# Optimization experiments

Hardware: AMD Instinct MI355X
Metric: run time of the kernel (lower is better)

Reference implementation:

```python
import jax, jax.numpy as jnp
import numpy as np

N = 100_000
E = 1_600_000
D_IN, D_H, D_L = 128, 64, 32


def _glorot(key, shape):
    fan_in, fan_out = shape[0], shape[1]
    s = jnp.sqrt(6.0 / (fan_in + fan_out)).astype(jnp.float32)
    return jax.random.uniform(key, shape, jnp.float32, -s, s)


def setup_inputs() -> dict:
    key = jax.random.key(0)
    ks = jax.random.split(key, 8)
    x = jax.random.normal(ks[0], (N, D_IN), jnp.float32)
    edge_index = jax.random.randint(ks[1], (2, E), 0, N, dtype=jnp.int64)
    return {
        "x": x,
        "edge_index": edge_index,
        "W1": _glorot(ks[2], (D_IN, D_H)),
        "b1": jnp.zeros((D_H,), jnp.float32),
        "W2": _glorot(ks[3], (D_H, D_L)),
        "b2": jnp.zeros((D_L,), jnp.float32),
        "Wd1": _glorot(ks[4], (D_L, D_H)),
        "bd1": jnp.zeros((D_H,), jnp.float32),
        "Wd2": _glorot(ks[5], (D_H, D_IN)),
        "bd2": jnp.zeros((D_IN,), jnp.float32),
    }


def gcn_conv(x, W, b, src, dst, num_nodes):
    """PyG GCNConv: add self-loops, symmetric normalization, aggregate, bias."""
    loop = jnp.arange(num_nodes, dtype=src.dtype)
    s = jnp.concatenate([src, loop])  # sources (message senders)
    d = jnp.concatenate([dst, loop])  # targets (message receivers)
    deg = jax.ops.segment_sum(jnp.ones_like(s, dtype=x.dtype), d, num_segments=num_nodes)
    dinv = jnp.where(deg > 0, jax.lax.rsqrt(deg), 0.0)
    norm = dinv[s] * dinv[d]                      # [E+N]
    h = x @ W                                     # [N, out] dense transform first
    msgs = h[s] * norm[:, None]                   # gather + scale, [E+N, out]
    out = jax.ops.segment_sum(msgs, d, num_segments=num_nodes)  # scatter-add
    return out + b


def reference(x, edge_index, W1, b1, W2, b2, Wd1, bd1, Wd2, bd2):
    src, dst = edge_index[0], edge_index[1]
    n = x.shape[0]
    z = gcn_conv(x, W1, b1, src, dst, n)
    z = jax.nn.relu(z)
    z = gcn_conv(z, W2, b2, src, dst, n)          # latent embedding
    h = jax.nn.relu(z @ Wd1 + bd1)
    reconstructed_x = h @ Wd2 + bd2
    return (reconstructed_x, z)
```

## Files before the change

### kernel.cpp

```cpp
#include <hip/hip_runtime.h>
#include <stdint.h>

#define N_NODES 100000
#define N_EDGES 1600000
#define D_INF   128
#define D_HID   64
#define D_LAT   32

typedef __attribute__((ext_vector_type(8))) short bf16x8;
typedef __attribute__((ext_vector_type(4))) float f32x4;
typedef __attribute__((ext_vector_type(8))) unsigned short u16x8;

__device__ __forceinline__ unsigned short f2bf(float v) {
  union { float f; unsigned int u; } x; x.f = v;
  unsigned int u = x.u + 0x7FFF + ((x.u >> 16) & 1);
  return (unsigned short)(u >> 16);
}
__device__ __forceinline__ float bf2f(unsigned short h) {
  union { unsigned int u; float f; } x; x.u = ((unsigned int)h) << 16;
  return x.f;
}


#define NBKT      196
#define BKT_SHIFT 9
#define BKT_CAP   10240
#define EPB       2048
#define ABLOCKS   782

__global__ __launch_bounds__(256) void k_binA(const int* __restrict__ esrc,
                                              const int* __restrict__ edst,
                                              int* __restrict__ bkcnt,
                                              int* __restrict__ stage) {
  __shared__ int cnt[NBKT];
  __shared__ int sc[256];
  __shared__ int garel[NBKT];
  __shared__ int pos[NBKT];
  __shared__ __align__(16) int2 stg[EPB];
  int t = threadIdx.x;
  int e0 = blockIdx.x * EPB;

  for (int i = t; i < NBKT; i += 256) cnt[i] = 0;
  __syncthreads();

  int ds[8], ss[8];
  const int4* s4 = (const int4*)esrc;
  const int4* d4 = (const int4*)edst;
#pragma unroll
  for (int i = 0; i < 2; i++) {
    int idx4 = (e0 >> 2) + i * 256 + t;
    int4 dd = make_int4(-1, -1, -1, -1);
    int4 sv = make_int4(0, 0, 0, 0);
    if (idx4 < N_EDGES / 4) { dd = d4[idx4]; sv = s4[idx4]; }
    ds[i*4+0] = dd.x; ds[i*4+1] = dd.y; ds[i*4+2] = dd.z; ds[i*4+3] = dd.w;
    ss[i*4+0] = sv.x; ss[i*4+1] = sv.y; ss[i*4+2] = sv.z; ss[i*4+3] = sv.w;
  }
#pragma unroll
  for (int j = 0; j < 8; j++)
    if (ds[j] >= 0) atomicAdd(&cnt[ds[j] >> BKT_SHIFT], 1);
  __syncthreads();

  int c = (t < NBKT) ? cnt[t] : 0;
  sc[t] = c;
  __syncthreads();
  int incl = c;
#pragma unroll
  for (int off = 1; off < 256; off <<= 1) {
    int x = (t >= off) ? sc[t - off] : 0;
    __syncthreads();
    incl += x;
    sc[t] = incl;
    __syncthreads();
  }
  if (t < NBKT) {
    int lb = incl - c;
    int gb = 0;
    if (c > 0) gb = t * BKT_CAP + atomicAdd(&bkcnt[t], c);
    garel[t] = gb - lb;
    pos[t]   = lb;
  }
  __syncthreads();

#pragma unroll
  for (int j = 0; j < 8; j++) {
    if (ds[j] >= 0) {
      int b  = ds[j] >> BKT_SHIFT;
      int lp = atomicAdd(&pos[b], 1);
      stg[lp] = make_int2(ss[j], ds[j]);
    }
  }
  __syncthreads();

  int nval = N_EDGES - e0; if (nval > EPB) nval = EPB;
  for (int i = t; i < nval; i += 256) {
    int2 e = stg[i];
    stage[garel[e.y >> BKT_SHIFT] + i] = (e.x << BKT_SHIFT) | (e.y & 511);
  }
}

__global__ __launch_bounds__(1024) void k_csr(const int* __restrict__ stage,
                                              const int* __restrict__ bkcnt,
                                              int* __restrict__ beg,
                                              int* __restrict__ cnt,
                                              float* __restrict__ dinv,
                                              int* __restrict__ csr4) {
  __shared__ int hist[512];
  __shared__ int scan[512];
  int b = blockIdx.x, t = threadIdx.x;
  if (t < 512) hist[t] = 0;
  __syncthreads();
  int n = bkcnt[b];
  int nlo = b << BKT_SHIFT;
  const int* reg = stage + (size_t)b * BKT_CAP;
  for (int i = t; i < n; i += 1024)
    atomicAdd(&hist[reg[i] & 511], 1);
  __syncthreads();
  int v = (t < 512) ? hist[t] : 0;
  if (t < 512) scan[t] = v;
  __syncthreads();
  int incl = v;
#pragma unroll
  for (int off = 1; off < 512; off <<= 1) {
    int x = (t >= off && t < 512) ? scan[t - off] : 0;
    __syncthreads();
    if (t < 512) { incl += x; scan[t] = incl; }
    __syncthreads();
  }
  if (t < 512) {
    int loc = incl - v;
    int node = nlo + t;
    if (node < N_NODES) {
      beg[node]  = b * BKT_CAP + loc;
      cnt[node]  = v;
      dinv[node] = rsqrtf((float)(v + 1));
    }
    scan[t] = loc;
  }
  __syncthreads();
  int* c4 = csr4 + (size_t)b * BKT_CAP;
  for (int i = t; i < n; i += 1024) {
    int e = reg[i];
    int slot = atomicAdd(&scan[e & 511], 1);
    c4[slot] = e >> BKT_SHIFT;
  }
}


__global__ void k_prep_w(const float* __restrict__ W1, const float* __restrict__ W2,
                         const float* __restrict__ Wd1, const float* __restrict__ Wd2,
                         unsigned short* __restrict__ w1hi, unsigned short* __restrict__ w1lo,
                         unsigned short* __restrict__ w2hi, unsigned short* __restrict__ w2lo,
                         unsigned short* __restrict__ wd1hi, unsigned short* __restrict__ wd1lo,
                         unsigned short* __restrict__ wd2hi, unsigned short* __restrict__ wd2lo,
                         int* __restrict__ bkcnt) {
  if (blockIdx.x == 4) {
    if (threadIdx.x < NBKT) bkcnt[threadIdx.x] = 0;
    return;
  }
  const float* src; unsigned short *hi, *lo; int K, M;
  switch (blockIdx.x) {
    case 0:  src = W1;  hi = w1hi;  lo = w1lo;  K = 128; M = 64;  break;
    case 1:  src = W2;  hi = w2hi;  lo = w2lo;  K = 64;  M = 32;  break;
    case 2:  src = Wd1; hi = wd1hi; lo = wd1lo; K = 32;  M = 64;  break;
    default: src = Wd2; hi = wd2hi; lo = wd2lo; K = 64;  M = 128; break;
  }
  int KP = K + 8;
  for (int i = threadIdx.x; i < K * M; i += 256) {
    int k = i / M, c = i % M;
    float v = src[i];
    unsigned short h = f2bf(v);
    hi[c * KP + k] = h;
    lo[c * KP + k] = f2bf(v - bf2f(h));
  }
}


template<int NODES, int K, int M>
__global__ __launch_bounds__(256) void k_mfma_gemm(const float* __restrict__ X,
                                                   const unsigned short* __restrict__ Bhi,
                                                   const unsigned short* __restrict__ Blo,
                                                   const float* __restrict__ dinv,
                                                   unsigned short* __restrict__ Y16) {
  constexpr int KP     = K + 8;
  constexpr int NSTRIP = M / 16;
  constexpr int KSTEPS = K / 32;
  constexpr int MTW    = (NODES / 16) * NSTRIP / 4;
  __shared__ __align__(16) unsigned short Ahi[NODES * KP];
  __shared__ __align__(16) unsigned short Alo[NODES * KP];

  int t = threadIdx.x;
  int node0 = blockIdx.x * NODES;

  for (int i = t; i < NODES * K / 4; i += 256) {
    int n = i / (K / 4), f4 = i % (K / 4);
    float4 v = make_float4(0.f, 0.f, 0.f, 0.f);
    if (node0 + n < N_NODES) v = ((const float4*)(X + (size_t)(node0 + n) * K))[f4];
    int base = n * KP + f4 * 4;
    float vv[4] = {v.x, v.y, v.z, v.w};
#pragma unroll
    for (int j = 0; j < 4; j++) {
      unsigned short h = f2bf(vv[j]);
      Ahi[base + j] = h;
      Alo[base + j] = f2bf(vv[j] - bf2f(h));
    }
  }
  __syncthreads();

  int w = t >> 6, lane = t & 63;
  int quad = lane >> 4, r16 = lane & 15;
  int strip = w % NSTRIP;

  bf16x8 bh[KSTEPS], bl[KSTEPS];
  const unsigned short* bp = Bhi + (strip * 16 + r16) * KP + quad * 8;
  const unsigned short* bq = Blo + (strip * 16 + r16) * KP + quad * 8;
#pragma unroll
  for (int ks = 0; ks < KSTEPS; ks++) {
    bh[ks] = *(const bf16x8*)(bp + ks * 32);
    bl[ks] = *(const bf16x8*)(bq + ks * 32);
  }

#pragma unroll
  for (int c = 0; c < MTW; c++) {
    int mt = (w / NSTRIP) * MTW + c;
    f32x4 acc = {0.f, 0.f, 0.f, 0.f};
    const unsigned short* ap = &Ahi[(mt * 16 + r16) * KP + quad * 8];
    const unsigned short* aq = &Alo[(mt * 16 + r16) * KP + quad * 8];
#pragma unroll
    for (int ks = 0; ks < KSTEPS; ks++) {
      bf16x8 ah = *(const bf16x8*)(ap + ks * 32);
      bf16x8 al = *(const bf16x8*)(aq + ks * 32);
      acc = __builtin_amdgcn_mfma_f32_16x16x32_bf16(ah, bh[ks], acc, 0, 0, 0);
      acc = __builtin_amdgcn_mfma_f32_16x16x32_bf16(ah, bl[ks], acc, 0, 0, 0);
      acc = __builtin_amdgcn_mfma_f32_16x16x32_bf16(al, bh[ks], acc, 0, 0, 0);
    }
    int gn  = node0 + mt * 16 + quad * 4;
    int col = strip * 16 + r16;
#pragma unroll
    for (int r = 0; r < 4; r++) {
      if (gn + r < N_NODES)
        Y16[(size_t)(gn + r) * M + col] = f2bf(acc[r] * dinv[gn + r]);
    }
  }
}


template<int FEAT, bool RELU>
__global__ __launch_bounds__(256) void k_aggregate(const unsigned short* __restrict__ H16,
                            const int* __restrict__ beg,
                            const int* __restrict__ cnt,
                            const int* __restrict__ csr4,
                            const float* __restrict__ dinv, const float* __restrict__ bias,
                            float* __restrict__ OUT) {
  constexpr int LPE    = FEAT / 8;
  constexpr int GROUPS = 64 / LPE;

  int node = blockIdx.x * 4 + (threadIdx.x >> 6);
  int lane = threadIdx.x & 63;
  if (node >= N_NODES) return;
  int bg = beg[node], end = bg + cnt[node];
  int g  = lane / LPE;
  int f8 = lane % LPE;

  float a0=0.f,a1=0.f,a2=0.f,a3=0.f,a4=0.f,a5=0.f,a6=0.f,a7=0.f;

  for (int p = bg; p < end; p += 4 * GROUPS) {
    int   sarr[4];
    float marr[4];
    u16x8 harr[4];
#pragma unroll
    for (int b4 = 0; b4 < 4; b4++) {
      int q = p + b4 * GROUPS + g;
      sarr[b4] = (q < end) ? csr4[q] : node;
      marr[b4] = (q < end) ? 1.f : 0.f;
    }
#pragma unroll
    for (int b4 = 0; b4 < 4; b4++)
      harr[b4] = *(const u16x8*)(H16 + (size_t)sarr[b4] * FEAT + f8 * 8);
#pragma unroll
    for (int b4 = 0; b4 < 4; b4++) {
      float m = marr[b4];
      u16x8 h = harr[b4];
      a0 += bf2f(h[0]) * m; a1 += bf2f(h[1]) * m;
      a2 += bf2f(h[2]) * m; a3 += bf2f(h[3]) * m;
      a4 += bf2f(h[4]) * m; a5 += bf2f(h[5]) * m;
      a6 += bf2f(h[6]) * m; a7 += bf2f(h[7]) * m;
    }
  }

#pragma unroll
  for (int off = LPE; off < 64; off <<= 1) {
    a0 += __shfl_xor(a0, off, 64);
    a1 += __shfl_xor(a1, off, 64);
    a2 += __shfl_xor(a2, off, 64);
    a3 += __shfl_xor(a3, off, 64);
    a4 += __shfl_xor(a4, off, 64);
    a5 += __shfl_xor(a5, off, 64);
    a6 += __shfl_xor(a6, off, 64);
    a7 += __shfl_xor(a7, off, 64);
  }

  if (g == 0) {
    float di = dinv[node];
    u16x8 hs = *(const u16x8*)(H16 + (size_t)node * FEAT + f8 * 8);
    float4 bv0 = *(const float4*)(bias + f8 * 8);
    float4 bv1 = *(const float4*)(bias + f8 * 8 + 4);
    a0 = (a0 + bf2f(hs[0])) * di + bv0.x;
    a1 = (a1 + bf2f(hs[1])) * di + bv0.y;
    a2 = (a2 + bf2f(hs[2])) * di + bv0.z;
    a3 = (a3 + bf2f(hs[3])) * di + bv0.w;
    a4 = (a4 + bf2f(hs[4])) * di + bv1.x;
    a5 = (a5 + bf2f(hs[5])) * di + bv1.y;
    a6 = (a6 + bf2f(hs[6])) * di + bv1.z;
    a7 = (a7 + bf2f(hs[7])) * di + bv1.w;
    if (RELU) {
      a0 = fmaxf(a0, 0.f); a1 = fmaxf(a1, 0.f);
      a2 = fmaxf(a2, 0.f); a3 = fmaxf(a3, 0.f);
      a4 = fmaxf(a4, 0.f); a5 = fmaxf(a5, 0.f);
      a6 = fmaxf(a6, 0.f); a7 = fmaxf(a7, 0.f);
    }
    float4 o0; o0.x = a0; o0.y = a1; o0.z = a2; o0.w = a3;
    float4 o1; o1.x = a4; o1.y = a5; o1.z = a6; o1.w = a7;
    *(float4*)(OUT + (size_t)node * FEAT + f8 * 8)     = o0;
    *(float4*)(OUT + (size_t)node * FEAT + f8 * 8 + 4) = o1;
  }
}


__global__ __launch_bounds__(256) void k_decoder_mfma(
    const float* __restrict__ Z,
    const unsigned short* __restrict__ B1hi, const unsigned short* __restrict__ B1lo,
    const float* __restrict__ bd1,
    const unsigned short* __restrict__ B2hi, const unsigned short* __restrict__ B2lo,
    const float* __restrict__ bd2, float* __restrict__ RECON) {
  constexpr int KP1 = 40;
  constexpr int KP2 = 72;
  __shared__ __align__(16) unsigned short Azhi[64 * KP1];
  __shared__ __align__(16) unsigned short Azlo[64 * KP1];
  __shared__ __align__(16) unsigned short H3hi[64 * KP2];
  __shared__ __align__(16) unsigned short H3lo[64 * KP2];
  int t = threadIdx.x;
  int node0 = blockIdx.x * 64;

  for (int i = t; i < 512; i += 256) {
    int n = i >> 3, f4 = i & 7;
    float4 v = make_float4(0.f, 0.f, 0.f, 0.f);
    if (node0 + n < N_NODES) v = ((const float4*)(Z + (size_t)(node0 + n) * 32))[f4];
    int base = n * KP1 + f4 * 4;
    float vv[4] = {v.x, v.y, v.z, v.w};
#pragma unroll
    for (int j = 0; j < 4; j++) {
      unsigned short h = f2bf(vv[j]);
      Azhi[base + j] = h;
      Azlo[base + j] = f2bf(vv[j] - bf2f(h));
    }
  }
  __syncthreads();

  int w = t >> 6, lane = t & 63;
  int quad = lane >> 4, r16 = lane & 15;

  {
    int col = w * 16 + r16;
    float bias1 = bd1[col];
    bf16x8 bh = *(const bf16x8*)(B1hi + col * KP1 + quad * 8);
    bf16x8 bl = *(const bf16x8*)(B1lo + col * KP1 + quad * 8);
#pragma unroll
    for (int m = 0; m < 4; m++) {
      bf16x8 ah = *(const bf16x8*)(Azhi + (m * 16 + r16) * KP1 + quad * 8);
      bf16x8 al = *(const bf16x8*)(Azlo + (m * 16 + r16) * KP1 + quad * 8);
      f32x4 acc = {0.f, 0.f, 0.f, 0.f};
      acc = __builtin_amdgcn_mfma_f32_16x16x32_bf16(ah, bh, acc, 0, 0, 0);
      acc = __builtin_amdgcn_mfma_f32_16x16x32_bf16(ah, bl, acc, 0, 0, 0);
      acc = __builtin_amdgcn_mfma_f32_16x16x32_bf16(al, bh, acc, 0, 0, 0);
#pragma unroll
      for (int r = 0; r < 4; r++) {
        int row = m * 16 + quad * 4 + r;
        float hv = fmaxf(acc[r] + bias1, 0.f);
        unsigned short h = f2bf(hv);
        H3hi[row * KP2 + col] = h;
        H3lo[row * KP2 + col] = f2bf(hv - bf2f(h));
      }
    }
  }
  __syncthreads();

#pragma unroll
  for (int sp = 0; sp < 2; sp++) {
    int strip = w + sp * 4;
    int col = strip * 16 + r16;
    float bias2 = bd2[col];
    const unsigned short* b2h = B2hi + col * KP2 + quad * 8;
    const unsigned short* b2l = B2lo + col * KP2 + quad * 8;
    bf16x8 bh0 = *(const bf16x8*)(b2h);
    bf16x8 bh1 = *(const bf16x8*)(b2h + 32);
    bf16x8 bl0 = *(const bf16x8*)(b2l);
    bf16x8 bl1 = *(const bf16x8*)(b2l + 32);
#pragma unroll
    for (int m = 0; m < 4; m++) {
      const unsigned short* ahp = H3hi + (m * 16 + r16) * KP2 + quad * 8;
      const unsigned short* alp = H3lo + (m * 16 + r16) * KP2 + quad * 8;
      bf16x8 ah0 = *(const bf16x8*)(ahp);
      bf16x8 ah1 = *(const bf16x8*)(ahp + 32);
      bf16x8 al0 = *(const bf16x8*)(alp);
      bf16x8 al1 = *(const bf16x8*)(alp + 32);
      f32x4 acc = {0.f, 0.f, 0.f, 0.f};
      acc = __builtin_amdgcn_mfma_f32_16x16x32_bf16(ah0, bh0, acc, 0, 0, 0);
      acc = __builtin_amdgcn_mfma_f32_16x16x32_bf16(ah1, bh1, acc, 0, 0, 0);
      acc = __builtin_amdgcn_mfma_f32_16x16x32_bf16(ah0, bl0, acc, 0, 0, 0);
      acc = __builtin_amdgcn_mfma_f32_16x16x32_bf16(ah1, bl1, acc, 0, 0, 0);
      acc = __builtin_amdgcn_mfma_f32_16x16x32_bf16(al0, bh0, acc, 0, 0, 0);
      acc = __builtin_amdgcn_mfma_f32_16x16x32_bf16(al1, bh1, acc, 0, 0, 0);
#pragma unroll
      for (int r = 0; r < 4; r++) {
        int n = node0 + m * 16 + quad * 4 + r;
        if (n < N_NODES) RECON[(size_t)n * 128 + col] = acc[r] + bias2;
      }
    }
  }
}


extern "C" void kernel_launch(void* const* d_in, const int* in_sizes, int n_in,
                              void* d_out, int out_size, void* d_ws, size_t ws_size,
                              hipStream_t stream) {
  const float* x    = (const float*)d_in[0];
  const int*   eidx = (const int*)d_in[1];
  const int*   esrc = eidx;
  const int*   edst = eidx + N_EDGES;
  const float* W1  = (const float*)d_in[2];
  const float* b1  = (const float*)d_in[3];
  const float* W2  = (const float*)d_in[4];
  const float* b2  = (const float*)d_in[5];
  const float* Wd1 = (const float*)d_in[6];
  const float* bd1 = (const float*)d_in[7];
  const float* Wd2 = (const float*)d_in[8];
  const float* bd2 = (const float*)d_in[9];

  float* recon = (float*)d_out;
  float* z     = (float*)d_out + (size_t)N_NODES * D_INF;
  int*            stage = (int*)recon;
  unsigned short* h1_16 = (unsigned short*)recon;
  float*          z1    = (float*)((char*)recon + 12800000);
  unsigned short* h2_16 = (unsigned short*)((char*)recon + 38400000);

  char* ws = (char*)d_ws;
  int*   beg    = (int*)(ws + 0);
  int*   cntn   = (int*)(ws + 409600);
  float* dinv   = (float*)(ws + 819200);
  int*   bkcnt  = (int*)(ws + 1228800);
  int*   csr4   = (int*)(ws + 1229824);
  unsigned short* w1hi  = (unsigned short*)(ws + 9257984);
  unsigned short* w1lo  = (unsigned short*)(ws + 9275392);
  unsigned short* w2hi  = (unsigned short*)(ws + 9292800);
  unsigned short* w2lo  = (unsigned short*)(ws + 9297408);
  unsigned short* wd1hi = (unsigned short*)(ws + 9302016);
  unsigned short* wd1lo = (unsigned short*)(ws + 9307136);
  unsigned short* wd2hi = (unsigned short*)(ws + 9312256);
  unsigned short* wd2lo = (unsigned short*)(ws + 9330688);

  k_prep_w<<<5, 256, 0, stream>>>(W1, W2, Wd1, Wd2, w1hi, w1lo, w2hi, w2lo,
                                  wd1hi, wd1lo, wd2hi, wd2lo, bkcnt);
  k_binA<<<ABLOCKS, 256, 0, stream>>>(esrc, edst, bkcnt, stage);
  k_csr<<<NBKT, 1024, 0, stream>>>(stage, bkcnt, beg, cntn, dinv, csr4);

  k_mfma_gemm<64, 128, 64><<<(N_NODES + 63) / 64, 256, 0, stream>>>(x, w1hi, w1lo, dinv, h1_16);
  k_aggregate<64, true><<<(N_NODES + 3) / 4, 256, 0, stream>>>(h1_16, beg, cntn, csr4, dinv, b1, z1);
  k_mfma_gemm<64, 64, 32><<<(N_NODES + 63) / 64, 256, 0, stream>>>(z1, w2hi, w2lo, dinv, h2_16);
  k_aggregate<32, false><<<(N_NODES + 3) / 4, 256, 0, stream>>>(h2_16, beg, cntn, csr4, dinv, b2, z);
  k_decoder_mfma<<<(N_NODES + 63) / 64, 256, 0, stream>>>(z, wd1hi, wd1lo, bd1,
                                                          wd2hi, wd2lo, bd2, recon);
}
```

Baseline: 291.1 us.

## Fuse aggregation with following GEMM and decoder into two kernels

Merges the first GCN aggregation with the second layer's dense transform, and the second aggregation with the MLP decoder. Aggregated rows go to shared memory instead of global memory, which removes the fp32 z1 write and read and the z reread between kernels. The h2 buffer moves into the workspace, and the bucket capacity shrinks to make room for it. In exchange, each block now handles 64 nodes with 4 waves looping over 16 rows each, which may lower gather parallelism and occupancy. The tighter bucket capacity could also overflow on skewed degree distributions.

```diff
diff --git a/kernel.cpp b/kernel.cpp
--- a/kernel.cpp
+++ b/kernel.cpp
@@ -24,7 +24,7 @@
 
 #define NBKT      196
 #define BKT_SHIFT 9
-#define BKT_CAP   10240
+#define BKT_CAP   9216
 #define EPB       2048
 #define ABLOCKS   782
 
@@ -244,126 +244,208 @@
 }
 
 
-template<int FEAT, bool RELU>
-__global__ __launch_bounds__(256) void k_aggregate(const unsigned short* __restrict__ H16,
-                            const int* __restrict__ beg,
-                            const int* __restrict__ cnt,
-                            const int* __restrict__ csr4,
-                            const float* __restrict__ dinv, const float* __restrict__ bias,
-                            float* __restrict__ OUT) {
-  constexpr int LPE    = FEAT / 8;
-  constexpr int GROUPS = 64 / LPE;
-
-  int node = blockIdx.x * 4 + (threadIdx.x >> 6);
-  int lane = threadIdx.x & 63;
-  if (node >= N_NODES) return;
-  int bg = beg[node], end = bg + cnt[node];
-  int g  = lane / LPE;
-  int f8 = lane % LPE;
-
-  float a0=0.f,a1=0.f,a2=0.f,a3=0.f,a4=0.f,a5=0.f,a6=0.f,a7=0.f;
-
-  for (int p = bg; p < end; p += 4 * GROUPS) {
-    int   sarr[4];
-    float marr[4];
-    u16x8 harr[4];
-#pragma unroll
-    for (int b4 = 0; b4 < 4; b4++) {
-      int q = p + b4 * GROUPS + g;
-      sarr[b4] = (q < end) ? csr4[q] : node;
-      marr[b4] = (q < end) ? 1.f : 0.f;
-    }
-#pragma unroll
-    for (int b4 = 0; b4 < 4; b4++)
-      harr[b4] = *(const u16x8*)(H16 + (size_t)sarr[b4] * FEAT + f8 * 8);
-#pragma unroll
-    for (int b4 = 0; b4 < 4; b4++) {
-      float m = marr[b4];
-      u16x8 h = harr[b4];
-      a0 += bf2f(h[0]) * m; a1 += bf2f(h[1]) * m;
-      a2 += bf2f(h[2]) * m; a3 += bf2f(h[3]) * m;
-      a4 += bf2f(h[4]) * m; a5 += bf2f(h[5]) * m;
-      a6 += bf2f(h[6]) * m; a7 += bf2f(h[7]) * m;
-    }
-  }
-
-#pragma unroll
-  for (int off = LPE; off < 64; off <<= 1) {
-    a0 += __shfl_xor(a0, off, 64);
-    a1 += __shfl_xor(a1, off, 64);
-    a2 += __shfl_xor(a2, off, 64);
-    a3 += __shfl_xor(a3, off, 64);
-    a4 += __shfl_xor(a4, off, 64);
-    a5 += __shfl_xor(a5, off, 64);
-    a6 += __shfl_xor(a6, off, 64);
-    a7 += __shfl_xor(a7, off, 64);
-  }
-
-  if (g == 0) {
-    float di = dinv[node];
-    u16x8 hs = *(const u16x8*)(H16 + (size_t)node * FEAT + f8 * 8);
-    float4 bv0 = *(const float4*)(bias + f8 * 8);
-    float4 bv1 = *(const float4*)(bias + f8 * 8 + 4);
-    a0 = (a0 + bf2f(hs[0])) * di + bv0.x;
-    a1 = (a1 + bf2f(hs[1])) * di + bv0.y;
-    a2 = (a2 + bf2f(hs[2])) * di + bv0.z;
-    a3 = (a3 + bf2f(hs[3])) * di + bv0.w;
-    a4 = (a4 + bf2f(hs[4])) * di + bv1.x;
-    a5 = (a5 + bf2f(hs[5])) * di + bv1.y;
-    a6 = (a6 + bf2f(hs[6])) * di + bv1.z;
-    a7 = (a7 + bf2f(hs[7])) * di + bv1.w;
-    if (RELU) {
-      a0 = fmaxf(a0, 0.f); a1 = fmaxf(a1, 0.f);
-      a2 = fmaxf(a2, 0.f); a3 = fmaxf(a3, 0.f);
-      a4 = fmaxf(a4, 0.f); a5 = fmaxf(a5, 0.f);
-      a6 = fmaxf(a6, 0.f); a7 = fmaxf(a7, 0.f);
-    }
-    float4 o0; o0.x = a0; o0.y = a1; o0.z = a2; o0.w = a3;
-    float4 o1; o1.x = a4; o1.y = a5; o1.z = a6; o1.w = a7;
-    *(float4*)(OUT + (size_t)node * FEAT + f8 * 8)     = o0;
-    *(float4*)(OUT + (size_t)node * FEAT + f8 * 8 + 4) = o1;
-  }
-}
-
-
-__global__ __launch_bounds__(256) void k_decoder_mfma(
-    const float* __restrict__ Z,
-    const unsigned short* __restrict__ B1hi, const unsigned short* __restrict__ B1lo,
+__global__ __launch_bounds__(256) void k_agg1_gemm2(
+    const unsigned short* __restrict__ H16,
+    const int* __restrict__ beg, const int* __restrict__ cnt,
+    const int* __restrict__ csr4,
+    const float* __restrict__ dinv, const float* __restrict__ bias,
+    const unsigned short* __restrict__ B2hi, const unsigned short* __restrict__ B2lo,
+    unsigned short* __restrict__ H2) {
+  constexpr int KP = 72;
+  __shared__ __align__(16) unsigned short Azhi[64 * KP];
+  __shared__ __align__(16) unsigned short Azlo[64 * KP];
+  int t = threadIdx.x, w = t >> 6, lane = t & 63;
+  int node0 = blockIdx.x * 64;
+  int g = lane >> 3, f8 = lane & 7;
+
+  for (int it = 0; it < 16; ++it) {
+    int row  = it * 4 + w;
+    int node = node0 + row;
+    float a0=0.f,a1=0.f,a2=0.f,a3=0.f,a4=0.f,a5=0.f,a6=0.f,a7=0.f;
+    if (node < N_NODES) {
+      int bg = beg[node], end = bg + cnt[node];
+      for (int p = bg; p < end; p += 32) {
+        int   sarr[4]; float marr[4]; u16x8 harr[4];
+#pragma unroll
+        for (int b4 = 0; b4 < 4; b4++) {
+          int q = p + b4 * 8 + g;
+          sarr[b4] = (q < end) ? csr4[q] : node;
+          marr[b4] = (q < end) ? 1.f : 0.f;
+        }
+#pragma unroll
+        for (int b4 = 0; b4 < 4; b4++)
+          harr[b4] = *(const u16x8*)(H16 + (size_t)sarr[b4] * 64 + f8 * 8);
+#pragma unroll
+        for (int b4 = 0; b4 < 4; b4++) {
+          float m = marr[b4]; u16x8 h = harr[b4];
+          a0 += bf2f(h[0]) * m; a1 += bf2f(h[1]) * m;
+          a2 += bf2f(h[2]) * m; a3 += bf2f(h[3]) * m;
+          a4 += bf2f(h[4]) * m; a5 += bf2f(h[5]) * m;
+          a6 += bf2f(h[6]) * m; a7 += bf2f(h[7]) * m;
+        }
+      }
+#pragma unroll
+      for (int off = 8; off < 64; off <<= 1) {
+        a0 += __shfl_xor(a0, off, 64); a1 += __shfl_xor(a1, off, 64);
+        a2 += __shfl_xor(a2, off, 64); a3 += __shfl_xor(a3, off, 64);
+        a4 += __shfl_xor(a4, off, 64); a5 += __shfl_xor(a5, off, 64);
+        a6 += __shfl_xor(a6, off, 64); a7 += __shfl_xor(a7, off, 64);
+      }
+    }
+    if (g == 0) {
+      float vals[8] = {0.f,0.f,0.f,0.f,0.f,0.f,0.f,0.f};
+      if (node < N_NODES) {
+        float di = dinv[node];
+        u16x8 hs = *(const u16x8*)(H16 + (size_t)node * 64 + f8 * 8);
+        float4 bv0 = *(const float4*)(bias + f8 * 8);
+        float4 bv1 = *(const float4*)(bias + f8 * 8 + 4);
+        vals[0] = fmaxf((a0 + bf2f(hs[0])) * di + bv0.x, 0.f);
+        vals[1] = fmaxf((a1 + bf2f(hs[1])) * di + bv0.y, 0.f);
+        vals[2] = fmaxf((a2 + bf2f(hs[2])) * di + bv0.z, 0.f);
+        vals[3] = fmaxf((a3 + bf2f(hs[3])) * di + bv0.w, 0.f);
+        vals[4] = fmaxf((a4 + bf2f(hs[4])) * di + bv1.x, 0.f);
+        vals[5] = fmaxf((a5 + bf2f(hs[5])) * di + bv1.y, 0.f);
+        vals[6] = fmaxf((a6 + bf2f(hs[6])) * di + bv1.z, 0.f);
+        vals[7] = fmaxf((a7 + bf2f(hs[7])) * di + bv1.w, 0.f);
+      }
+      int base = row * KP + f8 * 8;
+#pragma unroll
+      for (int j = 0; j < 8; j++) {
+        unsigned short h = f2bf(vals[j]);
+        Azhi[base + j] = h;
+        Azlo[base + j] = f2bf(vals[j] - bf2f(h));
+      }
+    }
+  }
+  __syncthreads();
+
+  int quad = lane >> 4, r16 = lane & 15;
+  int strip = w & 1;
+  const unsigned short* bp = B2hi + (strip * 16 + r16) * KP + quad * 8;
+  const unsigned short* bq = B2lo + (strip * 16 + r16) * KP + quad * 8;
+  bf16x8 bh0 = *(const bf16x8*)(bp);
+  bf16x8 bh1 = *(const bf16x8*)(bp + 32);
+  bf16x8 bl0 = *(const bf16x8*)(bq);
+  bf16x8 bl1 = *(const bf16x8*)(bq + 32);
+#pragma unroll
+  for (int c = 0; c < 2; ++c) {
+    int mt = (w >> 1) * 2 + c;
+    const unsigned short* ap = &Azhi[(mt * 16 + r16) * KP + quad * 8];
+    const unsigned short* aq = &Azlo[(mt * 16 + r16) * KP + quad * 8];
+    bf16x8 ah0 = *(const bf16x8*)(ap);
+    bf16x8 ah1 = *(const bf16x8*)(ap + 32);
+    bf16x8 al0 = *(const bf16x8*)(aq);
+    bf16x8 al1 = *(const bf16x8*)(aq + 32);
+    f32x4 acc = {0.f, 0.f, 0.f, 0.f};
+    acc = __builtin_amdgcn_mfma_f32_16x16x32_bf16(ah0, bh0, acc, 0, 0, 0);
+    acc = __builtin_amdgcn_mfma_f32_16x16x32_bf16(ah1, bh1, acc, 0, 0, 0);
+    acc = __builtin_amdgcn_mfma_f32_16x16x32_bf16(ah0, bl0, acc, 0, 0, 0);
+    acc = __builtin_amdgcn_mfma_f32_16x16x32_bf16(ah1, bl1, acc, 0, 0, 0);
+    acc = __builtin_amdgcn_mfma_f32_16x16x32_bf16(al0, bh0, acc, 0, 0, 0);
+    acc = __builtin_amdgcn_mfma_f32_16x16x32_bf16(al1, bh1, acc, 0, 0, 0);
+    int gn  = node0 + mt * 16 + quad * 4;
+    int col = strip * 16 + r16;
+#pragma unroll
+    for (int r = 0; r < 4; r++) {
+      if (gn + r < N_NODES)
+        H2[(size_t)(gn + r) * 32 + col] = f2bf(acc[r] * dinv[gn + r]);
+    }
+  }
+}
+
+
+__global__ __launch_bounds__(256) void k_agg2_dec(
+    const unsigned short* __restrict__ H2,
+    const int* __restrict__ beg, const int* __restrict__ cnt,
+    const int* __restrict__ csr4,
+    const float* __restrict__ dinv, const float* __restrict__ bias,
+    const unsigned short* __restrict__ D1hi, const unsigned short* __restrict__ D1lo,
     const float* __restrict__ bd1,
-    const unsigned short* __restrict__ B2hi, const unsigned short* __restrict__ B2lo,
-    const float* __restrict__ bd2, float* __restrict__ RECON) {
+    const unsigned short* __restrict__ D2hi, const unsigned short* __restrict__ D2lo,
+    const float* __restrict__ bd2,
+    float* __restrict__ Z, float* __restrict__ RECON) {
   constexpr int KP1 = 40;
   constexpr int KP2 = 72;
   __shared__ __align__(16) unsigned short Azhi[64 * KP1];
   __shared__ __align__(16) unsigned short Azlo[64 * KP1];
   __shared__ __align__(16) unsigned short H3hi[64 * KP2];
   __shared__ __align__(16) unsigned short H3lo[64 * KP2];
-  int t = threadIdx.x;
+  int t = threadIdx.x, w = t >> 6, lane = t & 63;
   int node0 = blockIdx.x * 64;
-
-  for (int i = t; i < 512; i += 256) {
-    int n = i >> 3, f4 = i & 7;
-    float4 v = make_float4(0.f, 0.f, 0.f, 0.f);
-    if (node0 + n < N_NODES) v = ((const float4*)(Z + (size_t)(node0 + n) * 32))[f4];
-    int base = n * KP1 + f4 * 4;
-    float vv[4] = {v.x, v.y, v.z, v.w};
-#pragma unroll
-    for (int j = 0; j < 4; j++) {
-      unsigned short h = f2bf(vv[j]);
-      Azhi[base + j] = h;
-      Azlo[base + j] = f2bf(vv[j] - bf2f(h));
-    }
-  }
-  __syncthreads();
-
-  int w = t >> 6, lane = t & 63;
+  int g = lane >> 2, f8 = lane & 3;
+
+  for (int it = 0; it < 16; ++it) {
+    int row  = it * 4 + w;
+    int node = node0 + row;
+    float a0=0.f,a1=0.f,a2=0.f,a3=0.f,a4=0.f,a5=0.f,a6=0.f,a7=0.f;
+    if (node < N_NODES) {
+      int bg = beg[node], end = bg + cnt[node];
+      for (int p = bg; p < end; p += 64) {
+        int   sarr[4]; float marr[4]; u16x8 harr[4];
+#pragma unroll
+        for (int b4 = 0; b4 < 4; b4++) {
+          int q = p + b4 * 16 + g;
+          sarr[b4] = (q < end) ? csr4[q] : node;
+          marr[b4] = (q < end) ? 1.f : 0.f;
+        }
+#pragma unroll
+        for (int b4 = 0; b4 < 4; b4++)
+          harr[b4] = *(const u16x8*)(H2 + (size_t)sarr[b4] * 32 + f8 * 8);
+#pragma unroll
+        for (int b4 = 0; b4 < 4; b4++) {
+          float m = marr[b4]; u16x8 h = harr[b4];
+          a0 += bf2f(h[0]) * m; a1 += bf2f(h[1]) * m;
+          a2 += bf2f(h[2]) * m; a3 += bf2f(h[3]) * m;
+          a4 += bf2f(h[4]) * m; a5 += bf2f(h[5]) * m;
+          a6 += bf2f(h[6]) * m; a7 += bf2f(h[7]) * m;
+        }
+      }
+#pragma unroll
+      for (int off = 4; off < 64; off <<= 1) {
+        a0 += __shfl_xor(a0, off, 64); a1 += __shfl_xor(a1, off, 64);
+        a2 += __shfl_xor(a2, off, 64); a3 += __shfl_xor(a3, off, 64);
+        a4 += __shfl_xor(a4, off, 64); a5 += __shfl_xor(a5, off, 64);
+        a6 += __shfl_xor(a6, off, 64); a7 += __shfl_xor(a7, off, 64);
+      }
+    }
+    if (g == 0) {
+      float vals[8] = {0.f,0.f,0.f,0.f,0.f,0.f,0.f,0.f};
+      if (node < N_NODES) {
+        float di = dinv[node];
+        u16x8 hs = *(const u16x8*)(H2 + (size_t)node * 32 + f8 * 8);
+        float4 bv0 = *(const float4*)(bias + f8 * 8);
+        float4 bv1 = *(const float4*)(bias + f8 * 8 + 4);
+        vals[0] = (a0 + bf2f(hs[0])) * di + bv0.x;
+        vals[1] = (a1 + bf2f(hs[1])) * di + bv0.y;
+        vals[2] = (a2 + bf2f(hs[2])) * di + bv0.z;
+        vals[3] = (a3 + bf2f(hs[3])) * di + bv0.w;
+        vals[4] = (a4 + bf2f(hs[4])) * di + bv1.x;
+        vals[5] = (a5 + bf2f(hs[5])) * di + bv1.y;
+        vals[6] = (a6 + bf2f(hs[6])) * di + bv1.z;
+        vals[7] = (a7 + bf2f(hs[7])) * di + bv1.w;
+        float4 o0; o0.x = vals[0]; o0.y = vals[1]; o0.z = vals[2]; o0.w = vals[3];
+        float4 o1; o1.x = vals[4]; o1.y = vals[5]; o1.z = vals[6]; o1.w = vals[7];
+        *(float4*)(Z + (size_t)node * 32 + f8 * 8)     = o0;
+        *(float4*)(Z + (size_t)node * 32 + f8 * 8 + 4) = o1;
+      }
+      int base = row * KP1 + f8 * 8;
+#pragma unroll
+      for (int j = 0; j < 8; j++) {
+        unsigned short h = f2bf(vals[j]);
+        Azhi[base + j] = h;
+        Azlo[base + j] = f2bf(vals[j] - bf2f(h));
+      }
+    }
+  }
+  __syncthreads();
+
   int quad = lane >> 4, r16 = lane & 15;
 
   {
     int col = w * 16 + r16;
     float bias1 = bd1[col];
-    bf16x8 bh = *(const bf16x8*)(B1hi + col * KP1 + quad * 8);
-    bf16x8 bl = *(const bf16x8*)(B1lo + col * KP1 + quad * 8);
+    bf16x8 bh = *(const bf16x8*)(D1hi + col * KP1 + quad * 8);
+    bf16x8 bl = *(const bf16x8*)(D1lo + col * KP1 + quad * 8);
 #pragma unroll
     for (int m = 0; m < 4; m++) {
       bf16x8 ah = *(const bf16x8*)(Azhi + (m * 16 + r16) * KP1 + quad * 8);
@@ -389,8 +471,8 @@
     int strip = w + sp * 4;
     int col = strip * 16 + r16;
     float bias2 = bd2[col];
-    const unsigned short* b2h = B2hi + col * KP2 + quad * 8;
-    const unsigned short* b2l = B2lo + col * KP2 + quad * 8;
+    const unsigned short* b2h = D2hi + col * KP2 + quad * 8;
+    const unsigned short* b2l = D2lo + col * KP2 + quad * 8;
     bf16x8 bh0 = *(const bf16x8*)(b2h);
     bf16x8 bh1 = *(const bf16x8*)(b2h + 32);
     bf16x8 bl0 = *(const bf16x8*)(b2l);
@@ -440,8 +522,6 @@
   float* z     = (float*)d_out + (size_t)N_NODES * D_INF;
   int*            stage = (int*)recon;
   unsigned short* h1_16 = (unsigned short*)recon;
-  float*          z1    = (float*)((char*)recon + 12800000);
-  unsigned short* h2_16 = (unsigned short*)((char*)recon + 38400000);
 
   char* ws = (char*)d_ws;
   int*   beg    = (int*)(ws + 0);
@@ -449,14 +529,15 @@
   float* dinv   = (float*)(ws + 819200);
   int*   bkcnt  = (int*)(ws + 1228800);
   int*   csr4   = (int*)(ws + 1229824);
-  unsigned short* w1hi  = (unsigned short*)(ws + 9257984);
-  unsigned short* w1lo  = (unsigned short*)(ws + 9275392);
-  unsigned short* w2hi  = (unsigned short*)(ws + 9292800);
-  unsigned short* w2lo  = (unsigned short*)(ws + 9297408);
-  unsigned short* wd1hi = (unsigned short*)(ws + 9302016);
-  unsigned short* wd1lo = (unsigned short*)(ws + 9307136);
-  unsigned short* wd2hi = (unsigned short*)(ws + 9312256);
-  unsigned short* wd2lo = (unsigned short*)(ws + 9330688);
+  unsigned short* w1hi  = (unsigned short*)(ws + 8455168);
+  unsigned short* w1lo  = (unsigned short*)(ws + 8472576);
+  unsigned short* w2hi  = (unsigned short*)(ws + 8489984);
+  unsigned short* w2lo  = (unsigned short*)(ws + 8494592);
+  unsigned short* wd1hi = (unsigned short*)(ws + 8499200);
+  unsigned short* wd1lo = (unsigned short*)(ws + 8504320);
+  unsigned short* wd2hi = (unsigned short*)(ws + 8509440);
+  unsigned short* wd2lo = (unsigned short*)(ws + 8527872);
+  unsigned short* h2_16 = (unsigned short*)(ws + 8546304);
 
   k_prep_w<<<5, 256, 0, stream>>>(W1, W2, Wd1, Wd2, w1hi, w1lo, w2hi, w2lo,
                                   wd1hi, wd1lo, wd2hi, wd2lo, bkcnt);
@@ -464,9 +545,9 @@
   k_csr<<<NBKT, 1024, 0, stream>>>(stage, bkcnt, beg, cntn, dinv, csr4);
 
   k_mfma_gemm<64, 128, 64><<<(N_NODES + 63) / 64, 256, 0, stream>>>(x, w1hi, w1lo, dinv, h1_16);
-  k_aggregate<64, true><<<(N_NODES + 3) / 4, 256, 0, stream>>>(h1_16, beg, cntn, csr4, dinv, b1, z1);
-  k_mfma_gemm<64, 64, 32><<<(N_NODES + 63) / 64, 256, 0, stream>>>(z1, w2hi, w2lo, dinv, h2_16);
-  k_aggregate<32, false><<<(N_NODES + 3) / 4, 256, 0, stream>>>(h2_16, beg, cntn, csr4, dinv, b2, z);
-  k_decoder_mfma<<<(N_NODES + 63) / 64, 256, 0, stream>>>(z, wd1hi, wd1lo, bd1,
-                                                          wd2hi, wd2lo, bd2, recon);
-}
+  k_agg1_gemm2<<<(N_NODES + 63) / 64, 256, 0, stream>>>(h1_16, beg, cntn, csr4, dinv, b1,
+                                                        w2hi, w2lo, h2_16);
+  k_agg2_dec<<<(N_NODES + 63) / 64, 256, 0, stream>>>(h2_16, beg, cntn, csr4, dinv, b2,
+                                                      wd1hi, wd1lo, bd1, wd2hi, wd2lo, bd2,
+                                                      z, recon);
+}
```

Result: slower. 326.6 us (+12.2%).
